# Optimization experiments

Measured on AMD Instinct MI355X. Metric: run time of the kernel, lower is better.

Reference implementation:

```python
import jax, jax.numpy as jnp
import numpy as np

B, T, D = 8, 1024, 1024
L = 512          # quantizer_latent_dim
V = 8192         # codebook_size
COMMIT = 0.25
PERP_COEF = 0.1


def _l2norm(v, axis=-1):
    return v * jax.lax.rsqrt(jnp.sum(v * v, axis=axis, keepdims=True) + 1e-12)


def _sq_dist(a, b):
    # ||a||^2 - 2 a.b + ||b||^2, a:[N,L] b:[V,L] -> [N,V]
    a2 = jnp.sum(a * a, axis=1, keepdims=True)
    b2 = jnp.sum(b * b, axis=1)[None, :]
    return a2 - 2.0 * jnp.einsum('nl,vl->nv', a, b) + b2


def setup_inputs() -> dict:
    key = jax.random.key(0)
    ks = jax.random.split(key, 4)
    x = jax.random.normal(ks[0], (B, T, D), dtype=jnp.float32)
    codebook = jax.random.normal(ks[1], (V, D), dtype=jnp.float32)
    W_in = jax.random.normal(ks[2], (D, L), dtype=jnp.float32) * (1.0 / np.sqrt(D))
    b_in = jnp.zeros((L,), dtype=jnp.float32)
    W_code = jax.random.normal(ks[3], (D, L), dtype=jnp.float32) * (1.0 / np.sqrt(D))
    b_code = jnp.zeros((L,), dtype=jnp.float32)
    return {"x": x, "codebook": codebook, "W_in": W_in, "b_in": b_in,
            "W_code": W_code, "b_code": b_code}


def _train_loss(quantized, x):
    e_latent = jnp.mean((jax.lax.stop_gradient(quantized) - x) ** 2) * COMMIT
    q_latent = jnp.mean((quantized - jax.lax.stop_gradient(x)) ** 2)
    return e_latent + q_latent


def reference(x, codebook, W_in, b_in, W_code, b_code):
    xf = x.reshape(-1, D)                                      # [N, D]
    latent_input = _l2norm(xf @ W_in + b_in)                   # [N, L]
    latent_code = _l2norm(codebook @ W_code + b_code)          # [V, L]
    sg_latent_code = jax.lax.stop_gradient(_l2norm(latent_code))
    distances = _sq_dist(latent_input, sg_latent_code).reshape(B, T, V)

    # approx_min_k with aggregate_to_topk (k = top_k_value = 1)
    idx = jax.lax.approx_min_k(distances, k=1, reduction_dimension=-1,
                               aggregate_to_topk=True)[1][..., 0]   # [B, T]
    encodings = jax.nn.one_hot(idx, V, dtype=x.dtype)          # [B, T, V]
    quantized = jnp.einsum('btv,vd->btd', encodings, codebook) # [B, T, D]

    codebook_usage = jnp.sum(jnp.sum(encodings, axis=(0, 1)) > 0) / V

    # train=True path: stop-grad quantized, straight-through estimator
    q_sg = jax.lax.stop_gradient(quantized)
    loss = _train_loss(q_sg, x)
    latent_quantized = q_sg @ W_code + b_code                  # code_to_latent(quantized)
    latent_x = x @ W_in + b_in                                 # input_to_latent(x)
    loss = loss + _train_loss(latent_quantized, latent_x)

    quantized_st = x + jax.lax.stop_gradient(q_sg - x)

    avg_probs = jnp.mean(encodings.reshape(-1, V), axis=0)
    log_perplexity = -jnp.sum(avg_probs * jnp.log(avg_probs + 1e-10))
    perplexity = jnp.exp(log_perplexity)
    loss = loss + PERP_COEF * log_perplexity

    return quantized_st, loss, perplexity, codebook_usage
```

## Files before the change

kernel.cpp:

```cpp
#include <hip/hip_runtime.h>
#include <hip/hip_bf16.h>
#include <stdint.h>

#define NTOK 8192
#define DDIM 1024
#define LDIM 512
#define VCB  8192
#define MROWS 16384

typedef unsigned long long u64;
typedef unsigned short ushort_t;
typedef unsigned char u8;
typedef float f32x4 __attribute__((ext_vector_type(4)));
typedef short s16x8 __attribute__((ext_vector_type(8)));

#define OFF_AB     0ull
#define OFF_QB     0ull
#define OFF_P      ((u64)MROWS * DDIM * 2)
#define OFF_QF     (OFF_P + (u64)MROWS * LDIM * 2)
#define OFF_WT     (OFF_QF + (u64)MROWS * 512)
#define OFF_B2     (OFF_WT + (u64)2 * LDIM * DDIM * 2)
#define OFF_B2B    (OFF_B2 + (u64)VCB * 4)
#define OFF_PART   (OFF_B2B + (u64)VCB * 4)
#define OFF_HIST   (OFF_PART + (u64)NTOK * 64 * 4)
#define OFF_PARTQ  (OFF_HIST + (u64)VCB * 4)
#define OFF_PARTL  (OFF_PARTQ + (u64)NTOK * 4)

__device__ __forceinline__ unsigned key_of(float f) {
  unsigned u = __float_as_uint(f);
  return (u & 0x80000000u) ? ~u : (u | 0x80000000u);
}

__device__ __forceinline__ ushort_t f2bf(float f) {
  unsigned u = __float_as_uint(f);
  unsigned r = (u + 0x7fffu + ((u >> 16) & 1u)) >> 16;
  return (ushort_t)r;
}
__device__ __forceinline__ float bf2f(unsigned b) {
  return __uint_as_float(b << 16);
}
__device__ __forceinline__ unsigned pkbf(float a, float b) {
  __hip_bfloat162 h = __float22bfloat162_rn(make_float2(a, b));
  unsigned r;
  __builtin_memcpy(&r, &h, 4);
  return r;
}

__device__ __forceinline__ void gload_lds16(const void* g, void* l) {
  __builtin_amdgcn_global_load_lds(
      (const __attribute__((address_space(1))) unsigned int*)g,
      (__attribute__((address_space(3))) unsigned int*)l, 16, 0, 0);
}

__device__ __forceinline__ f32x4 mfma16(s16x8 a, s16x8 b, f32x4 c) {
  return __builtin_amdgcn_mfma_f32_16x16x32_bf16(a, b, c, 0, 0, 0);
}
__device__ __forceinline__ f32x4 mfma8(u64 a, u64 b, f32x4 c) {
  return __builtin_amdgcn_mfma_f32_16x16x32_fp8_fp8((long long)a, (long long)b,
                                                    c, 0, 0, 0);
}

__global__ __launch_bounds__(256)
void k_wt(const float* __restrict__ Wi, const float* __restrict__ Wc,
          ushort_t* __restrict__ Wt, int* __restrict__ hist) {
  __shared__ float tile[32][33];
  const int tx = threadIdx.x, ty = threadIdx.y;
  const int t = ty * 32 + tx;
  const int lb = blockIdx.z * 512 + blockIdx.y * 32 + blockIdx.x;
  if (lb < 32) hist[lb * 256 + t] = 0;
  const float* W = blockIdx.z ? Wc : Wi;
  ushort_t* O = Wt + (blockIdx.z ? (size_t)LDIM * DDIM : 0);
  const int k0 = blockIdx.x * 32, n0 = blockIdx.y * 32;
#pragma unroll
  for (int i = 0; i < 4; ++i)
    tile[ty * 4 + i][tx] = W[(size_t)(k0 + ty * 4 + i) * LDIM + n0 + tx];
  __syncthreads();
#pragma unroll
  for (int i = 0; i < 4; ++i)
    O[(size_t)(n0 + ty * 4 + i) * DDIM + k0 + tx] = f2bf(tile[tx][ty * 4 + i]);
}

__global__ __launch_bounds__(256)
void k_cast(const float* __restrict__ x, const float* __restrict__ cb,
            ushort_t* __restrict__ Ab) {
  size_t i = ((size_t)blockIdx.x * 256 + threadIdx.x) * 8;
  const size_t half = (size_t)NTOK * DDIM;
  const float* src = (i < half) ? (x + i) : (cb + (i - half));
  float4 a = *(const float4*)src;
  float4 b = *(const float4*)(src + 4);
  uint4 o = make_uint4(pkbf(a.x, a.y), pkbf(a.z, a.w),
                       pkbf(b.x, b.y), pkbf(b.z, b.w));
  *(uint4*)&Ab[i] = o;
}

__global__ __launch_bounds__(256)
void k_latent(const ushort_t* __restrict__ Ab, const ushort_t* __restrict__ Wt,
              const float* __restrict__ bi, const float* __restrict__ bc,
              ushort_t* __restrict__ Pb) {
  __shared__ __align__(16) ushort_t As[128 * 32];
  __shared__ __align__(16) ushort_t Bs[128 * 32];
  const int t = threadIdx.x;
  const int wave = t >> 6, lane = t & 63;
  const int col0 = blockIdx.x * 128;
  const int m0 = blockIdx.y * 128;
  const bool isCode = (m0 >= NTOK);
  const u8* A = (const u8*)(Ab + (size_t)m0 * DDIM);
  const u8* W = (const u8*)(Wt + (isCode ? (size_t)LDIM * DDIM : 0) +
                            (size_t)col0 * DDIM);
  const float* bias = isCode ? bc : bi;

  const int srow = lane >> 2;
  const int rA = wave * 16 + srow;
  const int rB = 64 + wave * 16 + srow;
  const size_t goA = (size_t)rA * 2048 +
                     (((lane & 3) ^ (rA & 3) ^ ((rA >> 2) & 3)) << 4);
  const size_t goB = (size_t)rB * 2048 +
                     (((lane & 3) ^ (rB & 3) ^ ((rB >> 2) & 3)) << 4);
  u8* lwA0 = (u8*)As + (wave * 16) * 64;
  u8* lwA1 = (u8*)As + (64 + wave * 16) * 64;
  u8* lwB0 = (u8*)Bs + (wave * 16) * 64;
  u8* lwB1 = (u8*)Bs + (64 + wave * 16) * 64;

  const int wm = wave >> 1, wn = wave & 1;
  const int m = lane & 15, q = lane >> 4;
  const int pq = (q ^ (m & 3) ^ ((m >> 2) & 3)) * 16;
  int roffA[4], roffB[4];
#pragma unroll
  for (int i = 0; i < 4; ++i) {
    roffA[i] = (wm * 64 + i * 16 + m) * 64 + pq;
    roffB[i] = (wn * 64 + i * 16 + m) * 64 + pq;
  }

  f32x4 acc[4][4];
#pragma unroll
  for (int i = 0; i < 4; ++i)
#pragma unroll
    for (int j = 0; j < 4; ++j) acc[i][j] = (f32x4)(0.f);

  for (int it = 0; it < DDIM / 32; ++it) {
    const size_t kb = (size_t)it * 64;
    __syncthreads();
    gload_lds16(A + goA + kb, lwA0);
    gload_lds16(A + goB + kb, lwA1);
    gload_lds16(W + goA + kb, lwB0);
    gload_lds16(W + goB + kb, lwB1);
    __syncthreads();
    s16x8 af[4], bfr[4];
#pragma unroll
    for (int i = 0; i < 4; ++i)
      af[i] = *(const s16x8*)((const u8*)As + roffA[i]);
#pragma unroll
    for (int j = 0; j < 4; ++j)
      bfr[j] = *(const s16x8*)((const u8*)Bs + roffB[j]);
#pragma unroll
    for (int i = 0; i < 4; ++i)
#pragma unroll
      for (int j = 0; j < 4; ++j)
        acc[i][j] = mfma16(af[i], bfr[j], acc[i][j]);
  }

  float bv[4];
#pragma unroll
  for (int j = 0; j < 4; ++j) bv[j] = bias[col0 + wn * 64 + j * 16 + m];
#pragma unroll
  for (int i = 0; i < 4; ++i)
#pragma unroll
    for (int j = 0; j < 4; ++j) {
      int col = col0 + wn * 64 + j * 16 + m;
#pragma unroll
      for (int reg = 0; reg < 4; ++reg) {
        int row = m0 + wm * 64 + i * 16 + q * 4 + reg;
        Pb[(size_t)row * LDIM + col] = f2bf(acc[i][j][reg] + bv[j]);
      }
    }
}

__global__ __launch_bounds__(256)
void k_rownorm(const ushort_t* __restrict__ P, u8* __restrict__ Qf,
               ushort_t* __restrict__ Qb, float* __restrict__ b2,
               float* __restrict__ b2b) {
  const int row = blockIdx.x;
  const int t = threadIdx.x;
  const int lane = t & 63, wid = t >> 6;
  __shared__ float red[4];
  __shared__ float2 red2[4];
  __shared__ float bcast;
  const int c = t >> 5;
  const int w = (2 * t) & 63;
  const int g = w >> 4, h = w & 15;
  const int k = c * 64 + ((h < 8) ? (g * 8 + h) : (32 + g * 8 + (h - 8)));
  unsigned pv = *(const unsigned*)&P[(size_t)row * LDIM + k];
  float v0 = bf2f(pv & 0xffffu), v1 = bf2f(pv >> 16);
  float s = fmaf(v0, v0, v1 * v1);
#pragma unroll
  for (int o = 32; o > 0; o >>= 1) s += __shfl_down(s, o, 64);
  if (lane == 0) red[wid] = s;
  __syncthreads();
  if (t == 0) {
    float tot = red[0] + red[1] + red[2] + red[3];
    bcast = (float)(1.0 / sqrt((double)tot + 1e-12));
  }
  __syncthreads();
  float rs = bcast;
  int p8 = __builtin_amdgcn_cvt_pk_fp8_f32(v0 * rs, v1 * rs, 0, false);
  ((ushort_t*)Qf)[(size_t)row * 256 + t] = (ushort_t)((unsigned)p8 & 0xFFFFu);
  unsigned qp = pkbf(v0 * rs, v1 * rs);
  *(unsigned*)&Qb[(size_t)row * LDIM + k] = qp;
  if (row >= NTOK) {
    float f0 = __builtin_amdgcn_cvt_f32_fp8(p8, 0);
    float f1 = __builtin_amdgcn_cvt_f32_fp8(p8, 1);
    float g0 = bf2f(qp & 0xffffu), g1 = bf2f(qp >> 16);
    float s8 = fmaf(f0, f0, f1 * f1);
    float sb = fmaf(g0, g0, g1 * g1);
#pragma unroll
    for (int o = 32; o > 0; o >>= 1) {
      s8 += __shfl_down(s8, o, 64);
      sb += __shfl_down(sb, o, 64);
    }
    __syncthreads();
    if (lane == 0) red2[wid] = make_float2(s8, sb);
    __syncthreads();
    if (t == 0) {
      b2[row - NTOK]  = red2[0].x + red2[1].x + red2[2].x + red2[3].x;
      b2b[row - NTOK] = red2[0].y + red2[1].y + red2[2].y + red2[3].y;
    }
  }
}

__global__ __launch_bounds__(256)
void k_dist(const u8* __restrict__ Qf, const float* __restrict__ b2,
            unsigned* __restrict__ part) {
  __shared__ __align__(16) u8 S[2][128 * 64];
  u8* As = S[0];
  u8* Bs = S[1];
  const int t = threadIdx.x;
  const int wave = t >> 6, lane = t & 63;
  const int v0 = blockIdx.x * 128;
  const int n0 = blockIdx.y * 128;
  const u8* Ga = Qf + (size_t)n0 * 512;
  const u8* Gb = Qf + (size_t)(NTOK + v0) * 512;

  const int srow = lane >> 2;
  const int rA = wave * 16 + srow;
  const int rB = 64 + wave * 16 + srow;
  const size_t goA = (size_t)rA * 512 +
                     (((lane & 3) ^ (rA & 3) ^ ((rA >> 2) & 3)) << 4);
  const size_t goB = (size_t)rB * 512 +
                     (((lane & 3) ^ (rB & 3) ^ ((rB >> 2) & 3)) << 4);
  u8* lwA0 = As + (wave * 16) * 64;
  u8* lwA1 = As + (64 + wave * 16) * 64;
  u8* lwB0 = Bs + (wave * 16) * 64;
  u8* lwB1 = Bs + (64 + wave * 16) * 64;

  const int wm = wave >> 1, wn = wave & 1;
  const int m = lane & 15, q = lane >> 4;
  int roffA[4], roffB[4];
#pragma unroll
  for (int i = 0; i < 4; ++i) {
    int fr = wm * 64 + i * 16 + m;
    roffA[i] = fr * 64 + ((q ^ (fr & 3) ^ ((fr >> 2) & 3)) << 4);
    fr = wn * 64 + i * 16 + m;
    roffB[i] = fr * 64 + ((q ^ (fr & 3) ^ ((fr >> 2) & 3)) << 4);
  }

  f32x4 acc[4][4];
#pragma unroll
  for (int i = 0; i < 4; ++i)
#pragma unroll
    for (int j = 0; j < 4; ++j) acc[i][j] = (f32x4)(0.f);

  for (int it = 0; it < 8; ++it) {
    const int k0 = it * 64;
    __syncthreads();
    gload_lds16(Ga + goA + k0, lwA0);
    gload_lds16(Ga + goB + k0, lwA1);
    gload_lds16(Gb + goA + k0, lwB0);
    gload_lds16(Gb + goB + k0, lwB1);
    __syncthreads();
    ulonglong2 av[4], bv[4];
#pragma unroll
    for (int i = 0; i < 4; ++i) av[i] = *(const ulonglong2*)(As + roffA[i]);
#pragma unroll
    for (int j = 0; j < 4; ++j) bv[j] = *(const ulonglong2*)(Bs + roffB[j]);
#pragma unroll
    for (int i = 0; i < 4; ++i)
#pragma unroll
      for (int j = 0; j < 4; ++j)
        acc[i][j] = mfma8(av[i].x, bv[j].x, acc[i][j]);
#pragma unroll
    for (int i = 0; i < 4; ++i)
#pragma unroll
      for (int j = 0; j < 4; ++j)
        acc[i][j] = mfma8(av[i].y, bv[j].y, acc[i][j]);
  }

  float b2v[4];
#pragma unroll
  for (int j = 0; j < 4; ++j) b2v[j] = b2[v0 + wn * 64 + j * 16 + m];

  __syncthreads();
  unsigned* tbl = (unsigned*)S;
#pragma unroll
  for (int i = 0; i < 4; ++i)
#pragma unroll
    for (int reg = 0; reg < 4; ++reg) {
      unsigned best = 0xFFFFFFFFu;
#pragma unroll
      for (int j = 0; j < 4; ++j) {
        float key = fmaf(-2.f, acc[i][j][reg], b2v[j]);
        unsigned pk = (key_of(key) & 0xFFFFE000u) |
                      (unsigned)(v0 + wn * 64 + j * 16 + m);
        best = (pk < best) ? pk : best;
      }
      int r = wm * 64 + i * 16 + q * 4 + reg;
      int slot = (wn * 16 + m) ^ ((r & 7) << 2);
      tbl[r * 32 + slot] = best;
    }
  __syncthreads();
  if (t < 128) {
    unsigned mn = 0xFFFFFFFFu;
#pragma unroll
    for (int cc = 0; cc < 8; ++cc) {
      int gc = (cc + t) & 7;
      int base = t * 32 + ((gc * 4) ^ ((t & 7) << 2));
      uint4 v = *(const uint4*)&tbl[base];
      unsigned a = (v.x < v.y) ? v.x : v.y;
      unsigned b = (v.z < v.w) ? v.z : v.w;
      a = (a < b) ? a : b;
      mn = (a < mn) ? a : mn;
    }
    part[(size_t)(n0 + t) * 64 + blockIdx.x] = mn;
  }
}

__global__ __launch_bounds__(256)
void k_gather(const unsigned* __restrict__ part, const float* __restrict__ cb,
              const float* __restrict__ x, const ushort_t* __restrict__ P,
              const ushort_t* __restrict__ Qb, const float* __restrict__ b2b,
              float* __restrict__ out, int* __restrict__ hist,
              float* __restrict__ partq, float* __restrict__ partl) {
  const int n = blockIdx.x;
  const int t = threadIdx.x;
  const int lane = t & 63, wid = t >> 6;
  __shared__ float qin[512];
  __shared__ unsigned cand[8];
  __shared__ unsigned wcand[8];
  __shared__ int sIdx;
  __shared__ float rq[4], rl[4];

  unsigned uq = ((const unsigned*)(Qb + (size_t)n * LDIM))[t];
  qin[2 * t] = bf2f(uq & 0xffffu);
  qin[2 * t + 1] = bf2f(uq >> 16);

  if (t < 64) {
    unsigned v = part[(size_t)n * 64 + t];
#pragma unroll
    for (int it = 0; it < 8; ++it) {
      unsigned mn = v;
#pragma unroll
      for (int msk = 1; msk < 64; msk <<= 1) {
        unsigned o = (unsigned)__shfl_xor((int)mn, msk, 64);
        mn = (o < mn) ? o : mn;
      }
      if (t == 0) cand[it] = mn;
      if (v == mn) v = 0xFFFFFFFFu;
    }
  }
  __syncthreads();

  const int c = t >> 5, sl = t & 31;
  const int cidx = (int)(cand[c] & 0x1FFFu);
  const unsigned* crow =
      (const unsigned*)(Qb + (size_t)(NTOK + cidx) * LDIM) + sl * 8;
  uint4 va = *(const uint4*)(crow);
  uint4 vb = *(const uint4*)(crow + 4);
  const float* qs = &qin[sl * 16];
  float dot = 0.f;
  dot = fmaf(bf2f(va.x & 0xffffu), qs[0], dot);
  dot = fmaf(bf2f(va.x >> 16),     qs[1], dot);
  dot = fmaf(bf2f(va.y & 0xffffu), qs[2], dot);
  dot = fmaf(bf2f(va.y >> 16),     qs[3], dot);
  dot = fmaf(bf2f(va.z & 0xffffu), qs[4], dot);
  dot = fmaf(bf2f(va.z >> 16),     qs[5], dot);
  dot = fmaf(bf2f(va.w & 0xffffu), qs[6], dot);
  dot = fmaf(bf2f(va.w >> 16),     qs[7], dot);
  dot = fmaf(bf2f(vb.x & 0xffffu), qs[8], dot);
  dot = fmaf(bf2f(vb.x >> 16),     qs[9], dot);
  dot = fmaf(bf2f(vb.y & 0xffffu), qs[10], dot);
  dot = fmaf(bf2f(vb.y >> 16),     qs[11], dot);
  dot = fmaf(bf2f(vb.z & 0xffffu), qs[12], dot);
  dot = fmaf(bf2f(vb.z >> 16),     qs[13], dot);
  dot = fmaf(bf2f(vb.w & 0xffffu), qs[14], dot);
  dot = fmaf(bf2f(vb.w >> 16),     qs[15], dot);
#pragma unroll
  for (int msk = 1; msk < 32; msk <<= 1) dot += __shfl_xor(dot, msk, 32);
  if (sl == 0) {
    float key = fmaf(-2.f, dot, b2b[cidx]);
    wcand[c] = (key_of(key) & 0xFFFFE000u) | (unsigned)cidx;
  }
  __syncthreads();
  if (t == 0) {
    unsigned mm = wcand[0];
#pragma unroll
    for (int i = 1; i < 8; ++i) mm = (wcand[i] < mm) ? wcand[i] : mm;
    int iv = (int)(mm & 0x1FFFu);
    sIdx = iv;
    atomicAdd(&hist[iv], 1);
  }
  __syncthreads();
  const int iv = sIdx;

  float4 qv = *(const float4*)&cb[(size_t)iv * DDIM + t * 4];
  float4 xv = *(const float4*)&x[(size_t)n * DDIM + t * 4];
  *(float4*)&out[(size_t)n * DDIM + t * 4] = qv;
  float d0 = qv.x - xv.x, d1 = qv.y - xv.y, d2 = qv.z - xv.z, d3 = qv.w - xv.w;
  float sq = d0 * d0 + d1 * d1 + d2 * d2 + d3 * d3;
  unsigned lq = *(const unsigned*)&P[(size_t)(NTOK + iv) * LDIM + t * 2];
  unsigned lx = *(const unsigned*)&P[(size_t)n * LDIM + t * 2];
  float e0 = bf2f(lq & 0xffffu) - bf2f(lx & 0xffffu);
  float e1 = bf2f(lq >> 16) - bf2f(lx >> 16);
  float sl2 = e0 * e0 + e1 * e1;
#pragma unroll
  for (int o = 32; o > 0; o >>= 1) {
    sq += __shfl_down(sq, o, 64);
    sl2 += __shfl_down(sl2, o, 64);
  }
  if (lane == 0) { rq[wid] = sq; rl[wid] = sl2; }
  __syncthreads();
  if (t == 0) {
    partq[n] = rq[0] + rq[1] + rq[2] + rq[3];
    partl[n] = rl[0] + rl[1] + rl[2] + rl[3];
  }
}

__global__ __launch_bounds__(1024)
void k_final(const int* __restrict__ hist, const float* __restrict__ partq,
             const float* __restrict__ partl, float* __restrict__ out) {
  const int t = threadIdx.x;
  const int lane = t & 63, wid = t >> 6;
  float perp = 0.f, usedf = 0.f, sq = 0.f, sl = 0.f;
  for (int v = t; v < VCB; v += 1024) {
    int h = hist[v];
    usedf += (h > 0) ? 1.f : 0.f;
    float p = (float)h * (1.f / (float)NTOK);
    perp -= p * logf(p + 1e-10f);
  }
  for (int n = t; n < NTOK; n += 1024) {
    sq += partq[n];
    sl += partl[n];
  }
#pragma unroll
  for (int o = 32; o > 0; o >>= 1) {
    perp  += __shfl_down(perp, o, 64);
    usedf += __shfl_down(usedf, o, 64);
    sq    += __shfl_down(sq, o, 64);
    sl    += __shfl_down(sl, o, 64);
  }
  __shared__ float red[16][4];
  if (lane == 0) {
    red[wid][0] = perp; red[wid][1] = usedf; red[wid][2] = sq; red[wid][3] = sl;
  }
  __syncthreads();
  if (t == 0) {
    float Pp = 0.f, U = 0.f, SQ = 0.f, SL = 0.f;
    for (int w = 0; w < 16; ++w) {
      Pp += red[w][0]; U += red[w][1]; SQ += red[w][2]; SL += red[w][3];
    }
    float mseq = SQ / (float)((size_t)NTOK * DDIM);
    float msel = SL / (float)((size_t)NTOK * LDIM);
    float loss = 1.25f * mseq + 1.25f * msel + 0.1f * Pp;
    out[(size_t)NTOK * DDIM + 0] = loss;
    out[(size_t)NTOK * DDIM + 1] = expf(Pp);
    out[(size_t)NTOK * DDIM + 2] = U / (float)VCB;
  }
}

extern "C" void kernel_launch(void* const* d_in, const int* in_sizes, int n_in,
                              void* d_out, int out_size, void* d_ws, size_t ws_size,
                              hipStream_t stream) {
  const float* x  = (const float*)d_in[0];
  const float* cb = (const float*)d_in[1];
  const float* Wi = (const float*)d_in[2];
  const float* bi = (const float*)d_in[3];
  const float* Wc = (const float*)d_in[4];
  const float* bc = (const float*)d_in[5];
  float* out = (float*)d_out;
  char* ws = (char*)d_ws;
  ushort_t* Ab   = (ushort_t*)(ws + OFF_AB);
  ushort_t* Qb   = (ushort_t*)(ws + OFF_QB);
  ushort_t* P    = (ushort_t*)(ws + OFF_P);
  u8*       Qf   = (u8*)(ws + OFF_QF);
  ushort_t* Wt   = (ushort_t*)(ws + OFF_WT);
  float*    b2   = (float*)(ws + OFF_B2);
  float*    b2b  = (float*)(ws + OFF_B2B);
  unsigned* part = (unsigned*)(ws + OFF_PART);
  int*      hist = (int*)(ws + OFF_HIST);
  float*    partq = (float*)(ws + OFF_PARTQ);
  float*    partl = (float*)(ws + OFF_PARTL);

  hipLaunchKernelGGL(k_wt, dim3(DDIM / 32, LDIM / 32, 2), dim3(32, 8), 0,
                     stream, Wi, Wc, Wt, hist);
  hipLaunchKernelGGL(k_cast, dim3((MROWS * DDIM) / (256 * 8)), dim3(256), 0,
                     stream, x, cb, Ab);
  hipLaunchKernelGGL(k_latent, dim3(LDIM / 128, MROWS / 128), dim3(256), 0,
                     stream, Ab, Wt, bi, bc, P);
  hipLaunchKernelGGL(k_rownorm, dim3(MROWS), dim3(256), 0, stream, P, Qf, Qb,
                     b2, b2b);
  hipLaunchKernelGGL(k_dist, dim3(VCB / 128, NTOK / 128), dim3(256), 0, stream,
                     Qf, b2, part);
  hipLaunchKernelGGL(k_gather, dim3(NTOK), dim3(256), 0, stream, part, cb, x,
                     P, Qb, b2b, out, hist, partq, partl);
  hipLaunchKernelGGL(k_final, dim3(1), dim3(1024), 0, stream, hist, partq,
                     partl, out);
}
```

Before: 268.3 us.

## Use MX-scaled 16x16x128 FP8 MFMA for distance GEMM with 128-wide K tiles

Replaces the 16x16x32 fp8 MFMA in the distance kernel with the gfx950 scaled 16x16x128 f8f6f4 MFMA using unit scales. The K tile grows to 128, the LDS tiles and XOR swizzle are reworked for 128-byte rows, and the row-normalize kernel now writes the fp8 layout in plain order. The goal is higher matrix throughput per instruction and fewer loop iterations and barriers, at the cost of double the LDS and more register pressure.

```diff
diff --git a/kernel.cpp b/kernel.cpp
--- a/kernel.cpp
+++ b/kernel.cpp
@@ -13,6 +13,7 @@
 typedef unsigned char u8;
 typedef float f32x4 __attribute__((ext_vector_type(4)));
 typedef short s16x8 __attribute__((ext_vector_type(8)));
+typedef int i32x8 __attribute__((ext_vector_type(8)));
 
 #define OFF_AB     0ull
 #define OFF_QB     0ull
@@ -55,9 +56,9 @@
 __device__ __forceinline__ f32x4 mfma16(s16x8 a, s16x8 b, f32x4 c) {
   return __builtin_amdgcn_mfma_f32_16x16x32_bf16(a, b, c, 0, 0, 0);
 }
-__device__ __forceinline__ f32x4 mfma8(u64 a, u64 b, f32x4 c) {
-  return __builtin_amdgcn_mfma_f32_16x16x32_fp8_fp8((long long)a, (long long)b,
-                                                    c, 0, 0, 0);
+__device__ __forceinline__ f32x4 mfma_mx(i32x8 a, i32x8 b, f32x4 c) {
+  return __builtin_amdgcn_mfma_scale_f32_16x16x128_f8f6f4(
+      a, b, c, 0, 0, 0, 0x7f7f7f7f, 0, 0x7f7f7f7f);
 }
 
 __global__ __launch_bounds__(256)
@@ -185,10 +186,7 @@
   __shared__ float red[4];
   __shared__ float2 red2[4];
   __shared__ float bcast;
-  const int c = t >> 5;
-  const int w = (2 * t) & 63;
-  const int g = w >> 4, h = w & 15;
-  const int k = c * 64 + ((h < 8) ? (g * 8 + h) : (32 + g * 8 + (h - 8)));
+  const int k = 2 * t;
   unsigned pv = *(const unsigned*)&P[(size_t)row * LDIM + k];
   float v0 = bf2f(pv & 0xffffu), v1 = bf2f(pv >> 16);
   float s = fmaf(v0, v0, v1 * v1);
@@ -230,7 +228,7 @@
 __global__ __launch_bounds__(256)
 void k_dist(const u8* __restrict__ Qf, const float* __restrict__ b2,
             unsigned* __restrict__ part) {
-  __shared__ __align__(16) u8 S[2][128 * 64];
+  __shared__ __align__(16) u8 S[2][128 * 128];
   u8* As = S[0];
   u8* Bs = S[1];
   const int t = threadIdx.x;
@@ -240,27 +238,29 @@
   const u8* Ga = Qf + (size_t)n0 * 512;
   const u8* Gb = Qf + (size_t)(NTOK + v0) * 512;
 
-  const int srow = lane >> 2;
-  const int rA = wave * 16 + srow;
-  const int rB = 64 + wave * 16 + srow;
-  const size_t goA = (size_t)rA * 512 +
-                     (((lane & 3) ^ (rA & 3) ^ ((rA >> 2) & 3)) << 4);
-  const size_t goB = (size_t)rB * 512 +
-                     (((lane & 3) ^ (rB & 3) ^ ((rB >> 2) & 3)) << 4);
-  u8* lwA0 = As + (wave * 16) * 64;
-  u8* lwA1 = As + (64 + wave * 16) * 64;
-  u8* lwB0 = Bs + (wave * 16) * 64;
-  u8* lwB1 = Bs + (64 + wave * 16) * 64;
+  const int srow8 = lane >> 3;
+  const int sslot = lane & 7;
+  size_t go[4];
+  u8 *lwA[4], *lwB[4];
+#pragma unroll
+  for (int p = 0; p < 4; ++p) {
+    const int r = wave * 32 + p * 8 + srow8;
+    go[p] = (size_t)r * 512 + (size_t)((sslot ^ (r & 7)) << 4);
+    lwA[p] = As + (wave * 32 + p * 8) * 128;
+    lwB[p] = Bs + (wave * 32 + p * 8) * 128;
+  }
 
   const int wm = wave >> 1, wn = wave & 1;
   const int m = lane & 15, q = lane >> 4;
-  int roffA[4], roffB[4];
+  int roffA[4][2], roffB[4][2];
 #pragma unroll
   for (int i = 0; i < 4; ++i) {
     int fr = wm * 64 + i * 16 + m;
-    roffA[i] = fr * 64 + ((q ^ (fr & 3) ^ ((fr >> 2) & 3)) << 4);
+    roffA[i][0] = fr * 128 + (((2 * q) ^ (fr & 7)) << 4);
+    roffA[i][1] = fr * 128 + (((2 * q + 1) ^ (fr & 7)) << 4);
     fr = wn * 64 + i * 16 + m;
-    roffB[i] = fr * 64 + ((q ^ (fr & 3) ^ ((fr >> 2) & 3)) << 4);
+    roffB[i][0] = fr * 128 + (((2 * q) ^ (fr & 7)) << 4);
+    roffB[i][1] = fr * 128 + (((2 * q + 1) ^ (fr & 7)) << 4);
   }
 
   f32x4 acc[4][4];
@@ -269,29 +269,38 @@
 #pragma unroll
     for (int j = 0; j < 4; ++j) acc[i][j] = (f32x4)(0.f);
 
-  for (int it = 0; it < 8; ++it) {
-    const int k0 = it * 64;
+  for (int it = 0; it < 4; ++it) {
+    const int k0 = it * 128;
     __syncthreads();
-    gload_lds16(Ga + goA + k0, lwA0);
-    gload_lds16(Ga + goB + k0, lwA1);
-    gload_lds16(Gb + goA + k0, lwB0);
-    gload_lds16(Gb + goB + k0, lwB1);
+#pragma unroll
+    for (int p = 0; p < 4; ++p) gload_lds16(Ga + go[p] + k0, lwA[p]);
+#pragma unroll
+    for (int p = 0; p < 4; ++p) gload_lds16(Gb + go[p] + k0, lwB[p]);
     __syncthreads();
-    ulonglong2 av[4], bv[4];
-#pragma unroll
-    for (int i = 0; i < 4; ++i) av[i] = *(const ulonglong2*)(As + roffA[i]);
-#pragma unroll
-    for (int j = 0; j < 4; ++j) bv[j] = *(const ulonglong2*)(Bs + roffB[j]);
+    i32x8 av[4], bv[4];
+#pragma unroll
+    for (int i = 0; i < 4; ++i) {
+      uint4 lo = *(const uint4*)(As + roffA[i][0]);
+      uint4 hi = *(const uint4*)(As + roffA[i][1]);
+      av[i][0] = (int)lo.x; av[i][1] = (int)lo.y;
+      av[i][2] = (int)lo.z; av[i][3] = (int)lo.w;
+      av[i][4] = (int)hi.x; av[i][5] = (int)hi.y;
+      av[i][6] = (int)hi.z; av[i][7] = (int)hi.w;
+    }
+#pragma unroll
+    for (int j = 0; j < 4; ++j) {
+      uint4 lo = *(const uint4*)(Bs + roffB[j][0]);
+      uint4 hi = *(const uint4*)(Bs + roffB[j][1]);
+      bv[j][0] = (int)lo.x; bv[j][1] = (int)lo.y;
+      bv[j][2] = (int)lo.z; bv[j][3] = (int)lo.w;
+      bv[j][4] = (int)hi.x; bv[j][5] = (int)hi.y;
+      bv[j][6] = (int)hi.z; bv[j][7] = (int)hi.w;
+    }
 #pragma unroll
     for (int i = 0; i < 4; ++i)
 #pragma unroll
       for (int j = 0; j < 4; ++j)
-        acc[i][j] = mfma8(av[i].x, bv[j].x, acc[i][j]);
-#pragma unroll
-    for (int i = 0; i < 4; ++i)
-#pragma unroll
-      for (int j = 0; j < 4; ++j)
-        acc[i][j] = mfma8(av[i].y, bv[j].y, acc[i][j]);
+        acc[i][j] = mfma_mx(av[i], bv[j], acc[i][j]);
   }
 
   float b2v[4];
```

After: 254.9 us. -5.0%, faster.
